# Kernel optimization log

Measured on AMD Instinct MI355X. Metric: run time of the kernel, lower is better.

The kernel has to match this reference:

```python
import jax, jax.numpy as jnp
import numpy as np

B, N, H, NH = 8, 1024, 512, 8
DK = H // NH


def setup_inputs() -> dict:
    key = jax.random.key(0)
    ks = jax.random.split(key, 6)
    x = jax.random.normal(ks[0], (B, N, H), dtype=jnp.float32)
    adj = jax.random.randint(ks[1], (B, N, N), 0, 2, dtype=jnp.int32)
    # ensure no all-zero row (self-loops) so softmax is well-defined
    adj = jnp.maximum(adj, jnp.eye(N, dtype=jnp.int32)[None])
    s = 1.0 / np.sqrt(H)
    Wq = jax.random.normal(ks[2], (H, H), dtype=jnp.float32) * s
    Wk = jax.random.normal(ks[3], (H, H), dtype=jnp.float32) * s
    Wv = jax.random.normal(ks[4], (H, H), dtype=jnp.float32) * s
    Wg = jax.random.normal(ks[5], (H, 2 * H), dtype=jnp.float32) * (1.0 / np.sqrt(2 * H))
    bg = jnp.zeros((H,), dtype=jnp.float32)
    return {"x": x, "adj": adj, "Wq": Wq, "Wk": Wk, "Wv": Wv, "Wg": Wg, "bg": bg}


def reference(x, adj, Wq, Wk, Wv, Wg, bg):
    b, n, h = x.shape
    # projections (nn.Linear: x @ W.T), split heads -> [b, n, nh, dk]
    q = (x @ Wq.T).reshape(b, n, NH, DK)
    k = (x @ Wk.T).reshape(b, n, NH, DK)
    v = (x @ Wv.T).reshape(b, n, NH, DK)
    # scaled masked attention: [b, nh, n, n]
    scores = jnp.einsum('bqhd,bkhd->bhqk', q, k) / jnp.sqrt(jnp.float32(DK))
    mask = (adj != 0)[:, None, :, :]
    scores = jnp.where(mask, scores, -jnp.inf)
    attn = jax.nn.softmax(scores, axis=-1)  # dropout p=0.0 -> identity
    c = jnp.einsum('bhqk,bkhd->bqhd', attn, v).reshape(b, n, h)
    # sigmoid gated residual combine
    gate = jax.nn.sigmoid(jnp.concatenate([c, x], axis=2) @ Wg.T + bg)
    return gate * x + (1.0 - gate) * c
```

## Files before the change

kernel.cpp:

```cpp
#include <hip/hip_runtime.h>
#include <math.h>

#define B_  8
#define N_  1024
#define H_  512
#define NH_ 8
#define DK_ 64
#define M_  (B_ * N_)

typedef __attribute__((ext_vector_type(4))) float f32x4;
typedef __attribute__((ext_vector_type(8))) short bf16x8;

__device__ __forceinline__ unsigned short f2bf(float f) {
    unsigned int u = __float_as_uint(f);
    u = (u + 0x7fffu + ((u >> 16) & 1u)) >> 16;
    return (unsigned short)u;
}

__device__ __forceinline__ float bf2f(unsigned short s) {
    return __uint_as_float(((unsigned int)s) << 16);
}

__device__ __forceinline__ float fexp2(float x) {
#if __has_builtin(__builtin_amdgcn_exp2f)
    return __builtin_amdgcn_exp2f(x);
#else
    return exp2f(x);
#endif
}

__device__ __forceinline__ void gload16(const unsigned short* g, unsigned short* l) {
    __builtin_amdgcn_global_load_lds(
        (const __attribute__((address_space(1))) void*)g,
        (__attribute__((address_space(3))) void*)l, 16, 0, 0);
}

__global__ __launch_bounds__(256) void prep_k(const float* __restrict__ x,
                                              const float* __restrict__ Wq,
                                              const float* __restrict__ Wk,
                                              const float* __restrict__ Wv,
                                              const float* __restrict__ Wg,
                                              const int*   __restrict__ adj,
                                              unsigned short* __restrict__ xb,
                                              unsigned short* __restrict__ wqb,
                                              unsigned short* __restrict__ wkb,
                                              unsigned short* __restrict__ wvb,
                                              unsigned short* __restrict__ wgb,
                                              unsigned long long* __restrict__ mb)
{
    int id = blockIdx.x;
    if (id >= 5376) {
        int row  = id - 5376;
        int wv   = threadIdx.x >> 6;
        int lane = threadIdx.x & 63;
        const int* arow = &adj[(size_t)row * N_];
        #pragma unroll
        for (int j = 0; j < 4; ++j) {
            int kt = wv * 4 + j;
            int val = arow[kt * 64 + lane];
            unsigned long long m = __ballot(val != 0);
            if (lane == 0) mb[(size_t)row * 16 + kt] = m;
        }
        return;
    }
    const float* src; unsigned short* dst; int off; float scale = 1.0f;
    if (id < 4096)      { src = x;  dst = xb;  off = id; }
    else if (id < 4352) { src = Wq; dst = wqb; off = id - 4096; scale = 0.18033688011112042f; }
    else if (id < 4608) { src = Wk; dst = wkb; off = id - 4352; }
    else if (id < 4864) { src = Wv; dst = wvb; off = id - 4608; }
    else                { src = Wg; dst = wgb; off = id - 4864; }
    size_t i = (size_t)off * 1024 + threadIdx.x * 4;
    float4 v = *(const float4*)&src[i];
    *(ushort4*)&dst[i] = make_ushort4(f2bf(v.x * scale), f2bf(v.y * scale),
                                      f2bf(v.z * scale), f2bf(v.w * scale));
}

__global__ __launch_bounds__(256, 3) void proj_k(const unsigned short* __restrict__ xb,
                                                 const unsigned short* __restrict__ Wqb,
                                                 const unsigned short* __restrict__ Wkb,
                                                 const unsigned short* __restrict__ Wvb,
                                                 unsigned short* __restrict__ qk,
                                                 unsigned short* __restrict__ vt)
{
    __shared__ __align__(16) unsigned short SMEM[17408];
    unsigned short* As = SMEM;
    unsigned short* Bs = SMEM + 8192;

    const int tid = threadIdx.x;
    const int lane = tid & 63, wv = tid >> 6;
    const int ln = lane & 15, quad = lane >> 4;
    const int wm = wv >> 1, wn = wv & 1;
    const int row0 = blockIdx.x * 128;
    const int w    = blockIdx.y >> 2;
    const int col0 = (blockIdx.y & 3) * 128;
    const unsigned short* W = (w == 0) ? Wqb : ((w == 1) ? Wkb : Wvb);
    f32x4 acc[4][4] = {};

    auto issue = [&](int t, int bi) {
        int kt = t * 32;
        #pragma unroll
        for (int i = 0; i < 2; ++i) {
            int c = tid + i * 256;
            int c4 = c >> 7, row = c & 127;
            gload16(&xb[(size_t)(row0 + row) * H_ + kt + c4 * 8], &As[bi * 4096 + c * 8]);
            gload16(&W [(size_t)(col0 + row) * H_ + kt + c4 * 8], &Bs[bi * 4096 + c * 8]);
        }
    };

    issue(0, 0);
    for (int t = 0; t < 16; ++t) {
        __syncthreads();
        if (t < 15) issue(t + 1, (t + 1) & 1);
        const unsigned short* Ac = &As[(t & 1) * 4096];
        const unsigned short* Bc = &Bs[(t & 1) * 4096];
        bf16x8 af[4], bf[4];
        #pragma unroll
        for (int u = 0; u < 4; ++u) {
            af[u] = *(const bf16x8*)&Ac[(quad * 128 + wm * 64 + u * 16 + ln) * 8];
            bf[u] = *(const bf16x8*)&Bc[(quad * 128 + wn * 64 + u * 16 + ln) * 8];
        }
        #pragma unroll
        for (int mt = 0; mt < 4; ++mt)
            #pragma unroll
            for (int nt = 0; nt < 4; ++nt)
                acc[mt][nt] = __builtin_amdgcn_mfma_f32_16x16x32_bf16(af[mt], bf[nt], acc[mt][nt], 0, 0, 0);
    }

    if (w < 2) {
        __syncthreads();
        unsigned short* Ts = SMEM;
        #pragma unroll
        for (int mt = 0; mt < 4; ++mt)
            #pragma unroll
            for (int nt = 0; nt < 4; ++nt)
                #pragma unroll
                for (int r = 0; r < 4; ++r) {
                    int m_local = wm * 64 + mt * 16 + quad * 4 + r;
                    int c_local = wn * 64 + nt * 16 + ln;
                    Ts[m_local * 136 + c_local] = f2bf(acc[mt][nt][r]);
                }
        __syncthreads();
        #pragma unroll
        for (int j = 0; j < 8; ++j) {
            int m = j * 16 + (tid >> 4);
            int c = (tid & 15) * 8;
            uint4 u = *(const uint4*)&Ts[m * 136 + c];
            *(uint4*)&qk[(size_t)(row0 + m) * (2 * H_) + w * H_ + col0 + c] = u;
        }
    } else {
        __syncthreads();
        unsigned short* Ts = SMEM;
        #pragma unroll
        for (int mt = 0; mt < 4; ++mt)
            #pragma unroll
            for (int nt = 0; nt < 4; ++nt) {
                int c_local = wn * 64 + nt * 16 + ln;
                int n_local = wm * 64 + mt * 16 + quad * 4;
                ushort4 u = make_ushort4(f2bf(acc[mt][nt][0]), f2bf(acc[mt][nt][1]),
                                         f2bf(acc[mt][nt][2]), f2bf(acc[mt][nt][3]));
                *(ushort4*)&Ts[c_local * 136 + n_local] = u;
            }
        __syncthreads();
        const int bb = row0 >> 10, n_base = row0 & (N_ - 1);
        #pragma unroll
        for (int j = 0; j < 8; ++j) {
            int c_local = (tid >> 4) + j * 16;
            int nc = (tid & 15) * 8;
            int cg = col0 + c_local;
            int head = cg >> 6, d = cg & 63;
            uint4 u = *(const uint4*)&Ts[c_local * 136 + nc];
            *(uint4*)&vt[((size_t)(bb * NH_ + head) * DK_ + d) * N_ + n_base + nc] = u;
        }
    }
}

__global__ __launch_bounds__(256, 3) void attn_k(const unsigned short* __restrict__ qk,
                                                 const unsigned short* __restrict__ Vt,
                                                 const unsigned long long* __restrict__ Mb,
                                                 unsigned short* __restrict__ Cmb)
{
    const int bh   = blockIdx.x & 63;
    const int qt   = blockIdx.x >> 6;
    const int b    = bh >> 3;
    const int head = bh & 7;

    __shared__ unsigned short Ks[2][4096];
    __shared__ unsigned short Vs[2][4096];
    __shared__ unsigned short Ps[4][2][16][72];

    const int tid = threadIdx.x;
    const int lane = tid & 63, wv = tid >> 6;
    const int ln = lane & 15, quad = lane >> 4;
    const int q0 = qt * 128 + wv * 32 + ln;
    const int q1 = q0 + 16;

    const unsigned short* Kbase = qk + H_ + head * DK_;
    const unsigned short* Vbase = Vt + (size_t)(b * NH_ + head) * DK_ * N_;

    bf16x8 bq[2][2];
    #pragma unroll
    for (int kk = 0; kk < 2; ++kk) {
        bq[0][kk] = *(const bf16x8*)&qk[(size_t)(b * N_ + q0) * (2 * H_) + head * DK_ + kk * 32 + quad * 8];
        bq[1][kk] = *(const bf16x8*)&qk[(size_t)(b * N_ + q1) * (2 * H_) + head * DK_ + kk * 32 + quad * 8];
    }

    bf16x8 ones;
    #pragma unroll
    for (int j = 0; j < 8; ++j) ones[j] = (short)0x3F80;

    f32x4 o[2][4] = {};
    f32x4 osum[2] = {};

    auto issue = [&](int t, int bi) {
        #pragma unroll
        for (int i = 0; i < 2; ++i) {
            int c = tid + i * 256;
            int c8 = c >> 6, row = c & 63;
            gload16(&Kbase[(size_t)(b * N_ + t * 64 + row) * (2 * H_) + c8 * 8], &Ks[bi][c * 8]);
            gload16(&Vbase[(size_t)row * N_ + t * 64 + c8 * 8], &Vs[bi][c * 8]);
        }
    };

    issue(0, 0);

    for (int t = 0; t < 16; ++t) {
        __syncthreads();
        if (t < 15) issue(t + 1, (t + 1) & 1);
        const unsigned short* Kc = Ks[t & 1];
        const unsigned short* Vc = Vs[t & 1];

        unsigned long long mq[2];
        mq[0] = Mb[(size_t)(b * N_ + q0) * 16 + t];
        mq[1] = Mb[(size_t)(b * N_ + q1) * 16 + t];

        f32x4 s[2][4] = {};
        __builtin_amdgcn_s_setprio(1);
        #pragma unroll
        for (int kk = 0; kk < 2; ++kk)
            #pragma unroll
            for (int nt = 0; nt < 4; ++nt) {
                bf16x8 ka = *(const bf16x8*)&Kc[((kk * 4 + quad) * 64 + nt * 16 + ln) * 8];
                s[0][nt] = __builtin_amdgcn_mfma_f32_16x16x32_bf16(ka, bq[0][kk], s[0][nt], 0, 0, 0);
                s[1][nt] = __builtin_amdgcn_mfma_f32_16x16x32_bf16(ka, bq[1][kk], s[1][nt], 0, 0, 0);
            }
        __builtin_amdgcn_s_setprio(0);

        #pragma unroll
        for (int g = 0; g < 2; ++g) {
            unsigned long long sh = mq[g] >> (quad * 4);
            #pragma unroll
            for (int nt = 0; nt < 4; ++nt) {
                unsigned int bn = (unsigned int)(sh >> (nt * 16)) & 0xFu;
                float p[4];
                #pragma unroll
                for (int r = 0; r < 4; ++r) {
                    float e = fexp2(s[g][nt][r]);
                    p[r] = (bn & (1u << r)) ? e : 0.f;
                }
                unsigned int d0 = __builtin_amdgcn_perm(__float_as_uint(p[1]), __float_as_uint(p[0]), 0x07060302u);
                unsigned int d1 = __builtin_amdgcn_perm(__float_as_uint(p[3]), __float_as_uint(p[2]), 0x07060302u);
                *(uint2*)&Ps[wv][g][ln][nt * 16 + quad * 4] = make_uint2(d0, d1);
            }
        }

        bf16x8 pb[2][2];
        #pragma unroll
        for (int g = 0; g < 2; ++g)
            #pragma unroll
            for (int kk = 0; kk < 2; ++kk)
                pb[g][kk] = *(const bf16x8*)&Ps[wv][g][ln][kk * 32 + quad * 8];

        __builtin_amdgcn_s_setprio(1);
        #pragma unroll
        for (int kk = 0; kk < 2; ++kk) {
            #pragma unroll
            for (int dt = 0; dt < 4; ++dt) {
                bf16x8 va = *(const bf16x8*)&Vc[((kk * 4 + quad) * 64 + dt * 16 + ln) * 8];
                o[0][dt] = __builtin_amdgcn_mfma_f32_16x16x32_bf16(va, pb[0][kk], o[0][dt], 0, 0, 0);
                o[1][dt] = __builtin_amdgcn_mfma_f32_16x16x32_bf16(va, pb[1][kk], o[1][dt], 0, 0, 0);
            }
            osum[0] = __builtin_amdgcn_mfma_f32_16x16x32_bf16(ones, pb[0][kk], osum[0], 0, 0, 0);
            osum[1] = __builtin_amdgcn_mfma_f32_16x16x32_bf16(ones, pb[1][kk], osum[1], 0, 0, 0);
        }
        __builtin_amdgcn_s_setprio(0);
    }

    #pragma unroll
    for (int g = 0; g < 2; ++g) {
        float inv = 1.f / osum[g][0];
        int qg = (g == 0) ? q0 : q1;
        #pragma unroll
        for (int dt = 0; dt < 4; ++dt) {
            ushort4 u = make_ushort4(f2bf(o[g][dt][0] * inv), f2bf(o[g][dt][1] * inv),
                                     f2bf(o[g][dt][2] * inv), f2bf(o[g][dt][3] * inv));
            *(ushort4*)&Cmb[(size_t)(b * N_ + qg) * H_ + head * DK_ + dt * 16 + quad * 4] = u;
        }
    }
}

__global__ __launch_bounds__(256, 3) void gate_k(const unsigned short* __restrict__ cmb,
                                                 const unsigned short* __restrict__ xb,
                                                 const unsigned short* __restrict__ Wgb,
                                                 const float* __restrict__ bgp,
                                                 float* __restrict__ out)
{
    __shared__ __align__(16) unsigned short GSM[24576];
    unsigned short* As = GSM;
    unsigned short* Bs = GSM + 16384;
    const int tid = threadIdx.x;
    const int lane = tid & 63, wv = tid >> 6;
    const int ln = lane & 15, quad = lane >> 4;
    const int wm = wv >> 1, wn = wv & 1;
    const int row0 = blockIdx.x * 128;
    const int col0 = blockIdx.y * 64;
    f32x4 acc[4][2] = {};

    auto issue = [&](int t, int bi) {
        const unsigned short* Asrc = (t < 8) ? cmb : xb;
        int ko = (t * 64) & (H_ - 1);
        #pragma unroll
        for (int i = 0; i < 4; ++i) {
            int c = tid + i * 256;
            int c8 = c >> 7, row = c & 127;
            gload16(&Asrc[(size_t)(row0 + row) * H_ + ko + c8 * 8], &As[bi * 8192 + c * 8]);
        }
        #pragma unroll
        for (int i = 0; i < 2; ++i) {
            int c = tid + i * 256;
            int c8 = c >> 6, row = c & 63;
            gload16(&Wgb[(size_t)(col0 + row) * (2 * H_) + t * 64 + c8 * 8], &Bs[bi * 4096 + c * 8]);
        }
    };

    issue(0, 0);
    for (int t = 0; t < 16; ++t) {
        __syncthreads();
        if (t < 15) issue(t + 1, (t + 1) & 1);
        const unsigned short* Ac = &As[(t & 1) * 8192];
        const unsigned short* Bc = &Bs[(t & 1) * 4096];
        #pragma unroll
        for (int kk = 0; kk < 2; ++kk) {
            bf16x8 af[4], bf[2];
            #pragma unroll
            for (int u = 0; u < 4; ++u)
                af[u] = *(const bf16x8*)&Ac[((kk * 4 + quad) * 128 + wm * 64 + u * 16 + ln) * 8];
            #pragma unroll
            for (int u = 0; u < 2; ++u)
                bf[u] = *(const bf16x8*)&Bc[((kk * 4 + quad) * 64 + wn * 32 + u * 16 + ln) * 8];
            #pragma unroll
            for (int mt = 0; mt < 4; ++mt)
                #pragma unroll
                for (int nt = 0; nt < 2; ++nt)
                    acc[mt][nt] = __builtin_amdgcn_mfma_f32_16x16x32_bf16(af[mt], bf[nt], acc[mt][nt], 0, 0, 0);
        }
    }

    __syncthreads();
    float* Tsf = (float*)GSM;
    #pragma unroll
    for (int mt = 0; mt < 4; ++mt)
        #pragma unroll
        for (int nt = 0; nt < 2; ++nt)
            #pragma unroll
            for (int r = 0; r < 4; ++r) {
                int m_local = wm * 64 + mt * 16 + quad * 4 + r;
                int c_local = wn * 32 + nt * 16 + ln;
                Tsf[m_local * 68 + c_local] = acc[mt][nt][r];
            }
    __syncthreads();

    const int cl = (tid & 15) * 4;
    const float4 bg4 = *(const float4*)&bgp[col0 + cl];
    #pragma unroll
    for (int j = 0; j < 8; ++j) {
        int m = j * 16 + (tid >> 4);
        f32x4 a = *(const f32x4*)&Tsf[m * 68 + cl];
        ushort4 xv4 = *(const ushort4*)&xb [(size_t)(row0 + m) * H_ + col0 + cl];
        ushort4 cv4 = *(const ushort4*)&cmb[(size_t)(row0 + m) * H_ + col0 + cl];
        float4 o;
        {
            float g0 = 1.f / (1.f + __expf(-(a[0] + bg4.x)));
            float g1 = 1.f / (1.f + __expf(-(a[1] + bg4.y)));
            float g2 = 1.f / (1.f + __expf(-(a[2] + bg4.z)));
            float g3 = 1.f / (1.f + __expf(-(a[3] + bg4.w)));
            o.x = g0 * bf2f(xv4.x) + (1.f - g0) * bf2f(cv4.x);
            o.y = g1 * bf2f(xv4.y) + (1.f - g1) * bf2f(cv4.y);
            o.z = g2 * bf2f(xv4.z) + (1.f - g2) * bf2f(cv4.z);
            o.w = g3 * bf2f(xv4.w) + (1.f - g3) * bf2f(cv4.w);
        }
        *(float4*)&out[(size_t)(row0 + m) * H_ + col0 + cl] = o;
    }
}

extern "C" void kernel_launch(void* const* d_in, const int* in_sizes, int n_in,
                              void* d_out, int out_size, void* d_ws, size_t ws_size,
                              hipStream_t stream)
{
    const float* x   = (const float*)d_in[0];
    const int*   adj = (const int*)  d_in[1];
    const float* Wq  = (const float*)d_in[2];
    const float* Wk  = (const float*)d_in[3];
    const float* Wv  = (const float*)d_in[4];
    const float* Wg  = (const float*)d_in[5];
    const float* bg  = (const float*)d_in[6];
    float* out = (float*)d_out;

    unsigned short* xb  = (unsigned short*)d_ws;
    unsigned short* wqb = xb  + (size_t)M_ * H_;
    unsigned short* wkb = wqb + (size_t)H_ * H_;
    unsigned short* wvb = wkb + (size_t)H_ * H_;
    unsigned short* wgb = wvb + (size_t)H_ * H_;
    unsigned short* qk  = wgb + (size_t)H_ * 2 * H_;
    unsigned short* vt  = qk  + (size_t)M_ * 2 * H_;
    unsigned short* cmb = vt  + (size_t)M_ * H_;
    unsigned long long* mb = (unsigned long long*)(cmb + (size_t)M_ * H_);

    prep_k<<<5376 + 8192, 256, 0, stream>>>(x, Wq, Wk, Wv, Wg, adj,
                                            xb, wqb, wkb, wvb, wgb, mb);

    proj_k<<<dim3(M_ / 128, 12), 256, 0, stream>>>(xb, wqb, wkb, wvb, qk, vt);

    attn_k<<<B_ * NH_ * (N_ / 128), 256, 0, stream>>>(qk, vt, mb, cmb);

    gate_k<<<dim3(M_ / 128, H_ / 64), 256, 0, stream>>>(cmb, xb, wgb, bg, out);
}
```

Before: 196.4 us.

## Triple-buffer global-to-LDS loads with partial vmcnt waits in all three kernels

Converts the double-buffered async global-to-LDS pipelines in the projection, attention and gate kernels to triple buffering. Two tiles are prefetched ahead, and a partial s_waitcnt vmcnt waits only for the current tile before the barrier, replacing a full __syncthreads drain. This is meant to hide more memory latency per iteration. In exchange LDS use rises and the attn and gate launch bounds drop from 3 to 2 blocks per CU, which may reduce occupancy. Correctness also depends on the hand-counted vmcnt values matching the loads actually issued, including the mask loads in attn.

```diff
diff --git a/kernel.cpp b/kernel.cpp
--- a/kernel.cpp
+++ b/kernel.cpp
@@ -82,9 +82,7 @@
                                                  unsigned short* __restrict__ qk,
                                                  unsigned short* __restrict__ vt)
 {
-    __shared__ __align__(16) unsigned short SMEM[17408];
-    unsigned short* As = SMEM;
-    unsigned short* Bs = SMEM + 8192;
+    __shared__ __align__(16) unsigned short SMEM[24576];
 
     const int tid = threadIdx.x;
     const int lane = tid & 63, wv = tid >> 6;
@@ -102,17 +100,21 @@
         for (int i = 0; i < 2; ++i) {
             int c = tid + i * 256;
             int c4 = c >> 7, row = c & 127;
-            gload16(&xb[(size_t)(row0 + row) * H_ + kt + c4 * 8], &As[bi * 4096 + c * 8]);
-            gload16(&W [(size_t)(col0 + row) * H_ + kt + c4 * 8], &Bs[bi * 4096 + c * 8]);
+            gload16(&xb[(size_t)(row0 + row) * H_ + kt + c4 * 8], &SMEM[bi * 8192 + c * 8]);
+            gload16(&W [(size_t)(col0 + row) * H_ + kt + c4 * 8], &SMEM[bi * 8192 + 4096 + c * 8]);
         }
     };
 
     issue(0, 0);
+    issue(1, 1);
     for (int t = 0; t < 16; ++t) {
-        __syncthreads();
-        if (t < 15) issue(t + 1, (t + 1) & 1);
-        const unsigned short* Ac = &As[(t & 1) * 4096];
-        const unsigned short* Bc = &Bs[(t & 1) * 4096];
+        if (t < 15) { asm volatile("s_waitcnt vmcnt(4)" ::: "memory"); }
+        else        { asm volatile("s_waitcnt vmcnt(0)" ::: "memory"); }
+        __builtin_amdgcn_s_barrier();
+        __builtin_amdgcn_sched_barrier(0);
+        if (t < 14) issue(t + 2, (t + 2) % 3);
+        const unsigned short* Ac = &SMEM[(t % 3) * 8192];
+        const unsigned short* Bc = Ac + 4096;
         bf16x8 af[4], bf[4];
         #pragma unroll
         for (int u = 0; u < 4; ++u) {
@@ -174,7 +176,7 @@
     }
 }
 
-__global__ __launch_bounds__(256, 3) void attn_k(const unsigned short* __restrict__ qk,
+__global__ __launch_bounds__(256, 2) void attn_k(const unsigned short* __restrict__ qk,
                                                  const unsigned short* __restrict__ Vt,
                                                  const unsigned long long* __restrict__ Mb,
                                                  unsigned short* __restrict__ Cmb)
@@ -184,8 +186,8 @@
     const int b    = bh >> 3;
     const int head = bh & 7;
 
-    __shared__ unsigned short Ks[2][4096];
-    __shared__ unsigned short Vs[2][4096];
+    __shared__ unsigned short Ks[3][4096];
+    __shared__ unsigned short Vs[3][4096];
     __shared__ unsigned short Ps[4][2][16][72];
 
     const int tid = threadIdx.x;
@@ -222,16 +224,21 @@
     };
 
     issue(0, 0);
+    issue(1, 1);
 
     for (int t = 0; t < 16; ++t) {
-        __syncthreads();
-        if (t < 15) issue(t + 1, (t + 1) & 1);
-        const unsigned short* Kc = Ks[t & 1];
-        const unsigned short* Vc = Vs[t & 1];
+        if (t < 15) { asm volatile("s_waitcnt vmcnt(4)" ::: "memory"); }
+        else        { asm volatile("s_waitcnt vmcnt(0)" ::: "memory"); }
+        __builtin_amdgcn_s_barrier();
+        __builtin_amdgcn_sched_barrier(0);
 
         unsigned long long mq[2];
         mq[0] = Mb[(size_t)(b * N_ + q0) * 16 + t];
         mq[1] = Mb[(size_t)(b * N_ + q1) * 16 + t];
+
+        if (t < 14) issue(t + 2, (t + 2) % 3);
+        const unsigned short* Kc = Ks[t % 3];
+        const unsigned short* Vc = Vs[t % 3];
 
         f32x4 s[2][4] = {};
         __builtin_amdgcn_s_setprio(1);
@@ -298,15 +305,13 @@
     }
 }
 
-__global__ __launch_bounds__(256, 3) void gate_k(const unsigned short* __restrict__ cmb,
+__global__ __launch_bounds__(256, 2) void gate_k(const unsigned short* __restrict__ cmb,
                                                  const unsigned short* __restrict__ xb,
                                                  const unsigned short* __restrict__ Wgb,
                                                  const float* __restrict__ bgp,
                                                  float* __restrict__ out)
 {
-    __shared__ __align__(16) unsigned short GSM[24576];
-    unsigned short* As = GSM;
-    unsigned short* Bs = GSM + 16384;
+    __shared__ __align__(16) unsigned short GSM[36864];
     const int tid = threadIdx.x;
     const int lane = tid & 63, wv = tid >> 6;
     const int ln = lane & 15, quad = lane >> 4;
@@ -322,22 +327,26 @@
         for (int i = 0; i < 4; ++i) {
             int c = tid + i * 256;
             int c8 = c >> 7, row = c & 127;
-            gload16(&Asrc[(size_t)(row0 + row) * H_ + ko + c8 * 8], &As[bi * 8192 + c * 8]);
+            gload16(&Asrc[(size_t)(row0 + row) * H_ + ko + c8 * 8], &GSM[bi * 12288 + c * 8]);
         }
         #pragma unroll
         for (int i = 0; i < 2; ++i) {
             int c = tid + i * 256;
             int c8 = c >> 6, row = c & 63;
-            gload16(&Wgb[(size_t)(col0 + row) * (2 * H_) + t * 64 + c8 * 8], &Bs[bi * 4096 + c * 8]);
+            gload16(&Wgb[(size_t)(col0 + row) * (2 * H_) + t * 64 + c8 * 8], &GSM[bi * 12288 + 8192 + c * 8]);
         }
     };
 
     issue(0, 0);
+    issue(1, 1);
     for (int t = 0; t < 16; ++t) {
-        __syncthreads();
-        if (t < 15) issue(t + 1, (t + 1) & 1);
-        const unsigned short* Ac = &As[(t & 1) * 8192];
-        const unsigned short* Bc = &Bs[(t & 1) * 4096];
+        if (t < 15) { asm volatile("s_waitcnt vmcnt(6)" ::: "memory"); }
+        else        { asm volatile("s_waitcnt vmcnt(0)" ::: "memory"); }
+        __builtin_amdgcn_s_barrier();
+        __builtin_amdgcn_sched_barrier(0);
+        if (t < 14) issue(t + 2, (t + 2) % 3);
+        const unsigned short* Ac = &GSM[(t % 3) * 12288];
+        const unsigned short* Bc = Ac + 8192;
         #pragma unroll
         for (int kk = 0; kk < 2; ++kk) {
             bf16x8 af[4], bf[2];
```

Result: no change. 196.2 us (-0.1%).
